# Optimization experiments

Hardware: AMD Instinct MI355X
Metric: run time of the kernel (lower is better)

## Reference

```python
import jax, jax.numpy as jnp
import numpy as np

B = 2048
IN_FEATURES = 512
OUT_FEATURES = 32768
S = 64.0   # arcface default scale
M = 0.5    # arcface default margin
EPS = 1e-7


def _l2_normalize(x, axis=-1):
    # matches torch F.normalize(p=2, eps=1e-12)
    n = jnp.sqrt(jnp.sum(x * x, axis=axis, keepdims=True))
    return x / jnp.maximum(n, 1e-12)


def setup_inputs() -> dict:
    key = jax.random.key(0)
    k1, k2, k3 = jax.random.split(key, 3)
    features = jax.random.normal(k1, (B, IN_FEATURES), dtype=jnp.float32)
    y_true = jax.random.randint(k2, (B,), 0, OUT_FEATURES)
    # xavier_uniform_ for weight of shape (out, in)
    limit = float(np.sqrt(6.0 / (OUT_FEATURES + IN_FEATURES)))
    weight = jax.random.uniform(k3, (OUT_FEATURES, IN_FEATURES), dtype=jnp.float32,
                                minval=-limit, maxval=limit)
    return {"features": features, "y_true": y_true, "weight": weight}


def reference(features, y_true, weight):
    f = _l2_normalize(features)            # [B, D]
    w = _l2_normalize(weight)              # [C, D]
    wf = jnp.einsum('bd,cd->bc', f, w)     # [B, C] cosine logits
    tgt = wf[jnp.arange(wf.shape[0]), y_true]  # [B]
    # arcface margin transform
    numerator = S * jnp.cos(jnp.arccos(jnp.clip(tgt, -1.0 + EPS, 1.0 - EPS)) + M)
    # sum of exp(s*wf) over all non-target classes = full sum minus target term
    excl_sum = jnp.sum(jnp.exp(S * wf), axis=1) - jnp.exp(S * tgt)
    denominator = jnp.exp(numerator) + excl_sum
    L = numerator - jnp.log(denominator)
    return -jnp.mean(L)
```

## Files before the change

### kernel.cpp

```cpp
#include <hip/hip_runtime.h>
#include <hip/hip_bf16.h>
#include <math.h>


#define BN 2048
#define DK 512
#define CN 32768

typedef __attribute__((ext_vector_type(4))) float floatx4;
typedef __attribute__((ext_vector_type(16))) float floatx16;
typedef __attribute__((ext_vector_type(2))) long longx2;
typedef __attribute__((ext_vector_type(4))) long longx4;
typedef __attribute__((ext_vector_type(8))) int intx8;

__device__ inline float dot4(floatx4 a, floatx4 b) {
  return a.x * b.x + a.y * b.y + a.z * b.z + a.w * b.w;
}

__device__ inline int pack_fp8x4(floatx4 v) {
  int r = __builtin_amdgcn_cvt_pk_fp8_f32(v.x, v.y, 0, false);
  r = __builtin_amdgcn_cvt_pk_fp8_f32(v.z, v.w, r, true);
  return r;
}

__device__ inline int permute16(int j) {
  return ((j >> 1) & 3) * 4 + (j >> 3) * 2 + (j & 1);
}

__device__ inline void async_ld16(const void* g, void* l) {
  __builtin_amdgcn_global_load_lds(
      (const __attribute__((address_space(1))) void*)g,
      (__attribute__((address_space(3))) void*)l, 16, 0, 0);
}

template <int CTRL>
__device__ inline float dpp_add(float v) {
  int t = __builtin_amdgcn_update_dpp(0, __float_as_int(v), CTRL, 0xf, 0xf,
                                      true);
  return v + __int_as_float(t);
}

__global__ void prep_kernel(const float* __restrict__ feat,
                            const int* __restrict__ y,
                            const float* __restrict__ w,
                            int* __restrict__ fb8,
                            int* __restrict__ wb8,
                            float* __restrict__ tgt,
                            float* __restrict__ rowsum) {
  const int wave = threadIdx.x >> 6;
  const int l = threadIdx.x & 63;
  const int d0 = ((l >> 4) * 16)       + permute16(l & 15);
  const int d1 = ((4 + (l >> 4)) * 16) + permute16(l & 15);
  if (blockIdx.x < 8192) {
    const int row = blockIdx.x * 4 + wave;
    const floatx4* src = (const floatx4*)(w + (size_t)row * DK);
    floatx4 v0 = src[l];
    floatx4 v1 = src[64 + l];
    float s = dot4(v0, v0) + dot4(v1, v1);
#pragma unroll
    for (int off = 1; off < 64; off <<= 1) s += __shfl_xor(s, off, 64);
    const float scale = 1.0f / fmaxf(sqrtf(s), 1e-12f);
    v0 *= scale; v1 *= scale;
    int* db = wb8 + (size_t)row * 128;
    db[d0] = pack_fp8x4(v0);
    db[d1] = pack_fp8x4(v1);
  } else {
    const int i = (blockIdx.x - 8192) * 4 + wave;
    const floatx4* src = (const floatx4*)(feat + (size_t)i * DK);
    floatx4 v0 = src[l];
    floatx4 v1 = src[64 + l];
    const int cls = y[i];
    const floatx4* wr = (const floatx4*)(w + (size_t)cls * DK);
    floatx4 w0 = wr[l], w1 = wr[64 + l];
    float s  = dot4(v0, v0) + dot4(v1, v1);
    float d  = dot4(v0, w0) + dot4(v1, w1);
    float wn = dot4(w0, w0) + dot4(w1, w1);
#pragma unroll
    for (int off = 1; off < 64; off <<= 1) {
      s  += __shfl_xor(s, off, 64);
      d  += __shfl_xor(d, off, 64);
      wn += __shfl_xor(wn, off, 64);
    }
    const float fscale = 1.0f / fmaxf(sqrtf(s), 1e-12f);
    v0 *= fscale; v1 *= fscale;
    int* db = fb8 + (size_t)i * 128;
    db[d0] = pack_fp8x4(v0);
    db[d1] = pack_fp8x4(v1);
    if (l == 0) {
      tgt[i] = d * fscale / fmaxf(sqrtf(wn), 1e-12f);
      rowsum[i] = 0.0f;
    }
  }
}

__launch_bounds__(512, 4)
__global__ void gemm_exp_kernel(const char* __restrict__ fb8,
                                const char* __restrict__ wb8,
                                float* __restrict__ rowsum) {
  __shared__ char Bs[2][2 * 128 * 64];
  __shared__ float lsum[128];

  const int tid  = threadIdx.x;
  const int wave = tid >> 6;
  const int lane = tid & 63;

  const int n = blockIdx.x;
  const int tileM = ((n >> 3) & 15) * 128;
  const int tileN = (((n >> 7) << 3) | (n & 7)) * 128;

  const int wm = (wave & 3) * 32;
  const int wn = (wave >> 2) * 64;

  if (tid < 128) lsum[tid] = 0.0f;

  floatx16 acc[2];
#pragma unroll
  for (int tj = 0; tj < 2; ++tj)
#pragma unroll
    for (int r = 0; r < 16; ++r)
      acc[tj][r] = 0.0f;

  const int rowL = tid >> 2;
  const int uL   = (tid & 3) ^ ((rowL >> 1) & 3);
  const char* gB = wb8 + (size_t)(tileN + rowL) * DK + uL * 16;
  const int ldsO = wave * 1024;

  const int r31 = lane & 31;
  const int q2  = (lane >> 5) * 2;
  const longx2* gA = (const longx2*)(fb8 + (size_t)(tileM + wm + r31) * DK
                                     + q2 * 16);

  int offB0[2], offB1[2];
#pragma unroll
  for (int tj = 0; tj < 2; ++tj) {
    const int row = wn + tj * 32 + r31;
    const int rot = (row >> 1) & 3;
    offB0[tj] = row * 64 + ((q2    ) ^ rot) * 16;
    offB1[tj] = row * 64 + ((q2 + 1) ^ rot) * 16;
  }

  longx2 apre[2][2][2];

  async_ld16(gB,      &Bs[0][ldsO]);
  async_ld16(gB + 64, &Bs[0][8192 + ldsO]);
  gB += 128;
  apre[0][0][0] = gA[0];  apre[0][0][1] = gA[1];
  apre[0][1][0] = gA[4];  apre[0][1][1] = gA[5];
  gA += 8;

#pragma unroll
  for (int it = 0; it < DK / 128; ++it) {
    const int cur = it & 1;
    __syncthreads();
    if (it < DK / 128 - 1) {
      const int nxt = cur ^ 1;
      async_ld16(gB,      &Bs[nxt][ldsO]);
      async_ld16(gB + 64, &Bs[nxt][8192 + ldsO]);
      gB += 128;
      apre[nxt][0][0] = gA[0];  apre[nxt][0][1] = gA[1];
      apre[nxt][1][0] = gA[4];  apre[nxt][1][1] = gA[5];
      gA += 8;
    }

#pragma unroll
    for (int ks = 0; ks < 2; ++ks) {
      const char* Bb = &Bs[cur][ks * 8192];
      intx8 a, b[2];
      a = (intx8)(longx4){apre[cur][ks][0].x, apre[cur][ks][0].y,
                          apre[cur][ks][1].x, apre[cur][ks][1].y};
#pragma unroll
      for (int tj = 0; tj < 2; ++tj) {
        longx2 lo = *(const longx2*)(Bb + offB0[tj]);
        longx2 hi = *(const longx2*)(Bb + offB1[tj]);
        b[tj] = (intx8)(longx4){lo.x, lo.y, hi.x, hi.y};
      }
#pragma unroll
      for (int tj = 0; tj < 2; ++tj)
        acc[tj] = __builtin_amdgcn_mfma_scale_f32_32x32x64_f8f6f4(
            a, b[tj], acc[tj],
            0, 0, 0, 0x7f7f7f7f, 0, 0x7f7f7f7f);
    }
  }

  const int qrow = (lane >> 5) * 4;
#pragma unroll
  for (int r = 0; r < 16; ++r) {
    float v = __expf(64.0f * acc[0][r]) + __expf(64.0f * acc[1][r]);
    v = dpp_add<0x111>(v);
    v = dpp_add<0x112>(v);
    v = dpp_add<0x114>(v);
    v = dpp_add<0x118>(v);
    v = dpp_add<0x142>(v);
    if ((lane & 31) == 31)
      atomicAdd(&lsum[wm + qrow + (r & 3) + 8 * (r >> 2)], v);
  }
  __syncthreads();
  if (tid < 128)
    atomicAdd(&rowsum[tileM + tid], lsum[tid]);
}

__global__ void loss_kernel(const float* __restrict__ tgt,
                            const float* __restrict__ rowsum,
                            float* __restrict__ out) {
  __shared__ float wsum[8];
  const int t = threadIdx.x;
  float sum = 0.f;
  const float cM = 0.87758256189037271f;
  const float sM = 0.47942553860420301f;
  for (int i = t; i < BN; i += 512) {
    const float tg_raw = tgt[i];
    const float tg = fminf(fmaxf(tg_raw, -1.f + 1e-7f), 1.f - 1e-7f);
    const float num = 64.f * (tg * cM - sqrtf(fmaxf(1.f - tg * tg, 0.f)) * sM);
    const float den = expf(num) + rowsum[i] - expf(64.f * tg_raw);
    sum += num - logf(den);
  }
#pragma unroll
  for (int off = 1; off < 64; off <<= 1) sum += __shfl_xor(sum, off, 64);
  if ((t & 63) == 0) wsum[t >> 6] = sum;
  __syncthreads();
  if (t == 0) {
    float tot = 0.f;
#pragma unroll
    for (int k = 0; k < 8; ++k) tot += wsum[k];
    out[0] = -tot * (1.0f / (float)BN);
  }
}

extern "C" void kernel_launch(void* const* d_in, const int* in_sizes, int n_in,
                              void* d_out, int out_size, void* d_ws, size_t ws_size,
                              hipStream_t stream) {
  const float* features = (const float*)d_in[0];
  const int*   y_true   = (const int*)d_in[1];
  const float* weight   = (const float*)d_in[2];
  float* out = (float*)d_out;

  char* ws = (char*)d_ws;
  char* wb8    = ws;
  char* fb8    = ws + 16777216;
  float* tgt    = (float*)(ws + 17825792);
  float* rowsum = (float*)(ws + 17833984);

  prep_kernel<<<8192 + 512, 256, 0, stream>>>(features, y_true, weight,
                                              (int*)fb8, (int*)wb8, tgt, rowsum);
  gemm_exp_kernel<<<4096, 512, 0, stream>>>(fb8, wb8, rowsum);
  loss_kernel<<<1, 512, 0, stream>>>(tgt, rowsum, out);
}
```

Before: 174.5 us.

## Keep full-K weight tile resident in LDS and stream pre-packed features per wave

The GEMM is restructured so each block loads a 64-class weight tile with the full K=512 into LDS once, then loops over 1024 feature rows in 64-row chunks per wave. The feature matrix is pre-packed by the prep kernel into an MFMA-fragment-friendly layout, so waves read it with coalesced 16-byte loads straight from global memory. This removes the per-K-step LDS double buffering and barriers, and drops the shared partial row-sum reduction in favour of global atomics. The costs are more global atomics on rowsum, fewer and larger blocks (1024 blocks of 256 threads), and re-reading all features from L2 in every block.

```diff
diff --git a/kernel.cpp b/kernel.cpp
--- a/kernel.cpp
+++ b/kernel.cpp
@@ -27,6 +27,13 @@
   return ((j >> 1) & 3) * 4 + (j >> 3) * 2 + (j & 1);
 }
 
+__device__ inline int fbp_idx(int c32, int D, int r31) {
+  const int s = D >> 4;
+  const int w = D & 15;
+  return ((c32 * 8 + s) * 2 + ((w >> 2) & 1)) * 256 + (w >> 3) * 128 +
+         r31 * 4 + (w & 3);
+}
+
 __device__ inline void async_ld16(const void* g, void* l) {
   __builtin_amdgcn_global_load_lds(
       (const __attribute__((address_space(1))) void*)g,
@@ -43,14 +50,14 @@
 __global__ void prep_kernel(const float* __restrict__ feat,
                             const int* __restrict__ y,
                             const float* __restrict__ w,
-                            int* __restrict__ fb8,
+                            int* __restrict__ fbp,
                             int* __restrict__ wb8,
                             float* __restrict__ tgt,
                             float* __restrict__ rowsum) {
   const int wave = threadIdx.x >> 6;
   const int l = threadIdx.x & 63;
-  const int d0 = ((l >> 4) * 16)       + permute16(l & 15);
-  const int d1 = ((4 + (l >> 4)) * 16) + permute16(l & 15);
+  const int D0 = ((l >> 4) * 16)       + permute16(l & 15);
+  const int D1 = ((4 + (l >> 4)) * 16) + permute16(l & 15);
   if (blockIdx.x < 8192) {
     const int row = blockIdx.x * 4 + wave;
     const floatx4* src = (const floatx4*)(w + (size_t)row * DK);
@@ -62,8 +69,8 @@
     const float scale = 1.0f / fmaxf(sqrtf(s), 1e-12f);
     v0 *= scale; v1 *= scale;
     int* db = wb8 + (size_t)row * 128;
-    db[d0] = pack_fp8x4(v0);
-    db[d1] = pack_fp8x4(v1);
+    db[D0] = pack_fp8x4(v0);
+    db[D1] = pack_fp8x4(v1);
   } else {
     const int i = (blockIdx.x - 8192) * 4 + wave;
     const floatx4* src = (const floatx4*)(feat + (size_t)i * DK);
@@ -83,9 +90,9 @@
     }
     const float fscale = 1.0f / fmaxf(sqrtf(s), 1e-12f);
     v0 *= fscale; v1 *= fscale;
-    int* db = fb8 + (size_t)i * 128;
-    db[d0] = pack_fp8x4(v0);
-    db[d1] = pack_fp8x4(v1);
+    const int c32 = i >> 5, r31 = i & 31;
+    fbp[fbp_idx(c32, D0, r31)] = pack_fp8x4(v0);
+    fbp[fbp_idx(c32, D1, r31)] = pack_fp8x4(v1);
     if (l == 0) {
       tgt[i] = d * fscale / fmaxf(sqrtf(wn), 1e-12f);
       rowsum[i] = 0.0f;
@@ -93,110 +100,120 @@
   }
 }
 
-__launch_bounds__(512, 4)
-__global__ void gemm_exp_kernel(const char* __restrict__ fb8,
+__launch_bounds__(256, 3)
+__global__ void gemm_exp_kernel(const char* __restrict__ fbp,
                                 const char* __restrict__ wb8,
                                 float* __restrict__ rowsum) {
-  __shared__ char Bs[2][2 * 128 * 64];
-  __shared__ float lsum[128];
+  __shared__ char Bs[64 * 512];
 
   const int tid  = threadIdx.x;
   const int wave = tid >> 6;
   const int lane = tid & 63;
 
-  const int n = blockIdx.x;
-  const int tileM = ((n >> 3) & 15) * 128;
-  const int tileN = (((n >> 7) << 3) | (n & 7)) * 128;
-
-  const int wm = (wave & 3) * 32;
-  const int wn = (wave >> 2) * 64;
-
-  if (tid < 128) lsum[tid] = 0.0f;
-
-  floatx16 acc[2];
-#pragma unroll
-  for (int tj = 0; tj < 2; ++tj)
-#pragma unroll
-    for (int r = 0; r < 16; ++r)
-      acc[tj][r] = 0.0f;
-
-  const int rowL = tid >> 2;
-  const int uL   = (tid & 3) ^ ((rowL >> 1) & 3);
-  const char* gB = wb8 + (size_t)(tileN + rowL) * DK + uL * 16;
-  const int ldsO = wave * 1024;
+  const int bid    = blockIdx.x;
+  const int xcd    = bid & 7;
+  const int mhalf  = (bid >> 3) & 1;
+  const int ngroup = bid >> 4;
+  const int ntile  = ngroup * 8 + xcd;
+  const size_t tileN = (size_t)ntile * 64;
+  const int mbase  = mhalf * 1024;
+
+#pragma unroll
+  for (int i = 0; i < 8; ++i) {
+    const int c = i * 256 + tid;
+    const int r = c >> 5;
+    const int j = (c & 31) ^ (r & 7);
+    async_ld16(wb8 + (tileN + r) * 512 + j * 16,
+               &Bs[i * 4096 + wave * 1024]);
+  }
+  __syncthreads();
 
   const int r31 = lane & 31;
   const int q2  = (lane >> 5) * 2;
-  const longx2* gA = (const longx2*)(fb8 + (size_t)(tileM + wm + r31) * DK
-                                     + q2 * 16);
-
-  int offB0[2], offB1[2];
+  const int qrow = (lane >> 5) * 4;
+
+  int offBlo[2], offBhi[2], sfl[2];
 #pragma unroll
   for (int tj = 0; tj < 2; ++tj) {
-    const int row = wn + tj * 32 + r31;
-    const int rot = (row >> 1) & 3;
-    offB0[tj] = row * 64 + ((q2    ) ^ rot) * 16;
-    offB1[tj] = row * 64 + ((q2 + 1) ^ rot) * 16;
-  }
-
-  longx2 apre[2][2][2];
-
-  async_ld16(gB,      &Bs[0][ldsO]);
-  async_ld16(gB + 64, &Bs[0][8192 + ldsO]);
-  gB += 128;
-  apre[0][0][0] = gA[0];  apre[0][0][1] = gA[1];
-  apre[0][1][0] = gA[4];  apre[0][1][1] = gA[5];
-  gA += 8;
-
-#pragma unroll
-  for (int it = 0; it < DK / 128; ++it) {
-    const int cur = it & 1;
-    __syncthreads();
-    if (it < DK / 128 - 1) {
-      const int nxt = cur ^ 1;
-      async_ld16(gB,      &Bs[nxt][ldsO]);
-      async_ld16(gB + 64, &Bs[nxt][8192 + ldsO]);
-      gB += 128;
-      apre[nxt][0][0] = gA[0];  apre[nxt][0][1] = gA[1];
-      apre[nxt][1][0] = gA[4];  apre[nxt][1][1] = gA[5];
-      gA += 8;
-    }
-
-#pragma unroll
-    for (int ks = 0; ks < 2; ++ks) {
-      const char* Bb = &Bs[cur][ks * 8192];
-      intx8 a, b[2];
-      a = (intx8)(longx4){apre[cur][ks][0].x, apre[cur][ks][0].y,
-                          apre[cur][ks][1].x, apre[cur][ks][1].y};
-#pragma unroll
-      for (int tj = 0; tj < 2; ++tj) {
-        longx2 lo = *(const longx2*)(Bb + offB0[tj]);
-        longx2 hi = *(const longx2*)(Bb + offB1[tj]);
-        b[tj] = (intx8)(longx4){lo.x, lo.y, hi.x, hi.y};
+    const int row = tj * 32 + r31;
+    offBlo[tj] = row * 512 + ((q2    ) ^ (row & 3)) * 16;
+    offBhi[tj] = row * 512 + ((q2 + 1) ^ (row & 3)) * 16;
+    sfl[tj]    = (row & 4) << 4;
+  }
+
+  for (int cc = 0; cc < 4; ++cc) {
+    const int chunk64 = cc * 4 + wave;
+    const char* gA00 = fbp + (size_t)(mhalf * 32 + chunk64 * 2) * 16384
+                       + lane * 16;
+    const char* gA01 = gA00 + 1024;
+    const char* gA10 = gA00 + 16384;
+    const char* gA11 = gA00 + 16384 + 1024;
+
+    longx2 apre[2][2][2];
+    apre[0][0][0] = *(const longx2*)(gA00);
+    apre[0][0][1] = *(const longx2*)(gA01);
+    apre[0][1][0] = *(const longx2*)(gA10);
+    apre[0][1][1] = *(const longx2*)(gA11);
+
+    floatx16 acc[2][2];
+#pragma unroll
+    for (int ti = 0; ti < 2; ++ti)
+#pragma unroll
+      for (int tj = 0; tj < 2; ++tj)
+#pragma unroll
+        for (int r = 0; r < 16; ++r)
+          acc[ti][tj][r] = 0.0f;
+
+#pragma unroll
+    for (int s = 0; s < 8; ++s) {
+      const int cur = s & 1;
+      if (s < 7) {
+        const int nxt = cur ^ 1;
+        apre[nxt][0][0] = *(const longx2*)(gA00 + (s + 1) * 2048);
+        apre[nxt][0][1] = *(const longx2*)(gA01 + (s + 1) * 2048);
+        apre[nxt][1][0] = *(const longx2*)(gA10 + (s + 1) * 2048);
+        apre[nxt][1][1] = *(const longx2*)(gA11 + (s + 1) * 2048);
       }
-#pragma unroll
-      for (int tj = 0; tj < 2; ++tj)
-        acc[tj] = __builtin_amdgcn_mfma_scale_f32_32x32x64_f8f6f4(
-            a, b[tj], acc[tj],
-            0, 0, 0, 0x7f7f7f7f, 0, 0x7f7f7f7f);
-    }
-  }
-
-  const int qrow = (lane >> 5) * 4;
-#pragma unroll
-  for (int r = 0; r < 16; ++r) {
-    float v = __expf(64.0f * acc[0][r]) + __expf(64.0f * acc[1][r]);
-    v = dpp_add<0x111>(v);
-    v = dpp_add<0x112>(v);
-    v = dpp_add<0x114>(v);
-    v = dpp_add<0x118>(v);
-    v = dpp_add<0x142>(v);
-    if ((lane & 31) == 31)
-      atomicAdd(&lsum[wm + qrow + (r & 3) + 8 * (r >> 2)], v);
-  }
-  __syncthreads();
-  if (tid < 128)
-    atomicAdd(&rowsum[tileM + tid], lsum[tid]);
+      const int so0 = (s * 64) ^ sfl[0];
+      const int so1 = (s * 64) ^ sfl[1];
+      longx2 blo0 = *(const longx2*)(Bs + offBlo[0] + so0);
+      longx2 bhi0 = *(const longx2*)(Bs + offBhi[0] + so0);
+      longx2 blo1 = *(const longx2*)(Bs + offBlo[1] + so1);
+      longx2 bhi1 = *(const longx2*)(Bs + offBhi[1] + so1);
+      intx8 a0 = (intx8)(longx4){apre[cur][0][0].x, apre[cur][0][0].y,
+                                 apre[cur][0][1].x, apre[cur][0][1].y};
+      intx8 a1 = (intx8)(longx4){apre[cur][1][0].x, apre[cur][1][0].y,
+                                 apre[cur][1][1].x, apre[cur][1][1].y};
+      intx8 b0 = (intx8)(longx4){blo0.x, blo0.y, bhi0.x, bhi0.y};
+      intx8 b1 = (intx8)(longx4){blo1.x, blo1.y, bhi1.x, bhi1.y};
+      acc[0][0] = __builtin_amdgcn_mfma_scale_f32_32x32x64_f8f6f4(
+          a0, b0, acc[0][0], 0, 0, 0, 0x7f7f7f7f, 0, 0x7f7f7f7f);
+      acc[0][1] = __builtin_amdgcn_mfma_scale_f32_32x32x64_f8f6f4(
+          a0, b1, acc[0][1], 0, 0, 0, 0x7f7f7f7f, 0, 0x7f7f7f7f);
+      acc[1][0] = __builtin_amdgcn_mfma_scale_f32_32x32x64_f8f6f4(
+          a1, b0, acc[1][0], 0, 0, 0, 0x7f7f7f7f, 0, 0x7f7f7f7f);
+      acc[1][1] = __builtin_amdgcn_mfma_scale_f32_32x32x64_f8f6f4(
+          a1, b1, acc[1][1], 0, 0, 0, 0x7f7f7f7f, 0, 0x7f7f7f7f);
+    }
+
+    const int mrow0 = mbase + chunk64 * 64;
+#pragma unroll
+    for (int ti = 0; ti < 2; ++ti) {
+#pragma unroll
+      for (int r = 0; r < 16; ++r) {
+        float v = __expf(64.0f * acc[ti][0][r]) +
+                  __expf(64.0f * acc[ti][1][r]);
+        v = dpp_add<0x111>(v);
+        v = dpp_add<0x112>(v);
+        v = dpp_add<0x114>(v);
+        v = dpp_add<0x118>(v);
+        v = dpp_add<0x142>(v);
+        if ((lane & 31) == 31)
+          atomicAdd(&rowsum[mrow0 + ti * 32 + qrow + (r & 3) + 8 * (r >> 2)],
+                    v);
+      }
+    }
+  }
 }
 
 __global__ void loss_kernel(const float* __restrict__ tgt,
@@ -236,12 +253,12 @@
 
   char* ws = (char*)d_ws;
   char* wb8    = ws;
-  char* fb8    = ws + 16777216;
+  char* fbp    = ws + 16777216;
   float* tgt    = (float*)(ws + 17825792);
   float* rowsum = (float*)(ws + 17833984);
 
   prep_kernel<<<8192 + 512, 256, 0, stream>>>(features, y_true, weight,
-                                              (int*)fb8, (int*)wb8, tgt, rowsum);
-  gemm_exp_kernel<<<4096, 512, 0, stream>>>(fb8, wb8, rowsum);
+                                              (int*)fbp, (int*)wb8, tgt, rowsum);
+  gemm_exp_kernel<<<1024, 256, 0, stream>>>(fbp, wb8, rowsum);
   loss_kernel<<<1, 512, 0, stream>>>(tgt, rowsum, out);
 }
```

Result: slower. 374.2 us (+114.4%).
